# Kernel tuning notes

Hardware: AMD Instinct MI355X
Metric: run time of the kernel (lower is better)

## Reference

```python
import jax, jax.numpy as jnp
import numpy as np

V_MAX = 3.0
FEATURE_CLAMP = 10.0
TOP_K = 1


def _green_diag(d):
    """Diagonal of G = (tridiag(sub=1, diag=d, super=1))^{-1} for each batch row.
    d: (B, N) complex64. Stable two-sided continued-fraction (Thomas-like) recurrences:
      L_i = d_i - 1/L_{i-1},  U_i = d_i - 1/U_{i+1},  G_ii = 1/(L_i + U_i - d_i).
    Sequential over N (vectorized over B) via lax.scan.
    """
    dT = d.T  # (N, B)

    def step(c, di):
        nc = di - 1.0 / c
        return nc, nc

    L0 = dT[0]
    _, Lr = jax.lax.scan(step, L0, dT[1:])
    L = jnp.concatenate([L0[None], Lr], axis=0)  # (N, B)

    dR = dT[::-1]
    U0 = dR[0]
    _, Ur = jax.lax.scan(step, U0, dR[1:])
    U = jnp.concatenate([U0[None], Ur], axis=0)[::-1]  # (N, B)

    return (1.0 / (L + U - dT)).T  # (B, N)


def setup_inputs() -> dict:
    key = jax.random.key(0)
    B, N, D, E, F = 4, 4096, 512, 4, 2048
    ks = jax.random.split(key, 8)
    s = lambda k, sh, sc: (jax.random.normal(k, sh, jnp.float32) * sc)
    return dict(
        x=jax.random.normal(ks[0], (B, N, D), jnp.float32),
        v_proj_w=s(ks[1], (1, D), D ** -0.5),
        v_proj_b=jnp.zeros((1,), jnp.float32),
        gamma=jnp.float32(0.0),
        epsilon_param=jnp.float32(1.0),
        gate_w=s(ks[2], (E, D), D ** -0.5),
        gate_b=jnp.zeros((E,), jnp.float32),
        w1=s(ks[3], (E, D, F), D ** -0.5),
        b1=jnp.zeros((E, F), jnp.float32),
        w2=s(ks[4], (E, F, D), F ** -0.5),
        b2=jnp.zeros((E, D), jnp.float32),
        out_w=s(ks[5], (D, 2), 0.5),
        out_b=jnp.zeros((D,), jnp.float32),
        bk_scale=jnp.ones((D,), jnp.float32),
    )


def reference(x, v_proj_w, v_proj_b, gamma, epsilon_param, gate_w, gate_b,
              w1, b1, w2, b2, out_w, out_b, bk_scale):
    # 1) scalar potential from tokens
    v = jnp.einsum('bnd,od->bno', x, v_proj_w)[..., 0] + v_proj_b[0]  # (B, N)
    v = jnp.clip(v, -V_MAX, V_MAX)

    # 2) gamma-shifted complex tridiagonal Green's function diagonal
    eps = jax.nn.softplus(epsilon_param) + 1e-6
    z = 1j * (eps + gamma)                       # complex64 scalar
    d = ((v - 2.0).astype(jnp.complex64) - z)    # he_diag - z, (B, N)
    G = _green_diag(d)                            # (B, N) complex
    feats = jnp.clip(jnp.stack([G.real, G.imag], axis=-1), -FEATURE_CLAMP, FEATURE_CLAMP)  # (B,N,2)

    # 3) sparse MoE FFN (top-1 routing, experts = Linear -> GELU -> Linear)
    logits = jnp.einsum('bnd,ed->bne', x, gate_w) + gate_b
    probs = jax.nn.softmax(logits, axis=-1)
    top_p, top_i = jax.lax.top_k(probs, TOP_K)
    top_w = top_p / jnp.sum(top_p, axis=-1, keepdims=True)
    wmask = jnp.sum(jax.nn.one_hot(top_i, probs.shape[-1], dtype=probs.dtype) * top_w[..., None], axis=-2)  # (B,N,E)

    h = jax.nn.gelu(jnp.einsum('bnd,edf->benf', x, w1) + b1[None, :, None, :], approximate=False)
    y = jnp.einsum('benf,efd->bend', h, w2) + b2[None, :, None, :]
    ffn_out = jnp.einsum('bne,bend->bnd', wmask, y)

    # 4) combine spectral features with FFN output
    spec_out = jnp.einsum('bnc,dc->bnd', feats, out_w) + out_b
    return ffn_out + bk_scale * spec_out
```

## Files before the change

kernel.cpp:

```cpp
#include <hip/hip_runtime.h>
#include <hip/hip_bf16.h>
#include <math.h>


typedef __bf16 bf16x8 __attribute__((ext_vector_type(8)));
typedef float  f32x4  __attribute__((ext_vector_type(4)));
typedef __attribute__((address_space(3))) __bf16 lbf16;

#define B_   4
#define N_   4096
#define D_   512
#define E_   4
#define F_   2048
#define T_   (B_*N_)
#define CAP_ T_
#define R256 68
#define RT128 (R256*2)
#define PADROWS (R256*256)

#define LGKM_BARRIER() asm volatile("s_waitcnt lgkmcnt(0)\n\ts_barrier" ::: "memory")

__device__ __forceinline__ void gload_lds16(const __bf16* g, lbf16* l) {
    __builtin_amdgcn_global_load_lds(
        (__attribute__((address_space(1))) void*)(void*)g,
        (__attribute__((address_space(3))) void*)l, 16, 0, 0);
}

__device__ __forceinline__ float fast_gelu(float x) {
    float u = 1.5957691216f * fmaf(0.044715f * x, x * x, x);
    return x / (1.0f + __expf(-u));
}

__device__ __forceinline__ void mfma_tile(const char* Ab, const char* Bb,
                                          int cs0, int cs1, f32x4 acc[4][4]) {
    #pragma unroll
    for (int ks = 0; ks < 2; ++ks) {
        int cs = ks ? cs1 : cs0;
        bf16x8 af[4], bfr[4];
        #pragma unroll
        for (int m = 0; m < 4; ++m)
            af[m] = *(const bf16x8*)(Ab + m * 2048 + cs);
        #pragma unroll
        for (int n = 0; n < 4; ++n)
            bfr[n] = *(const bf16x8*)(Bb + n * 2048 + cs);
        #pragma unroll
        for (int m = 0; m < 4; ++m)
            #pragma unroll
            for (int n = 0; n < 4; ++n)
                acc[m][n] = __builtin_amdgcn_mfma_f32_16x16x32_bf16(af[m], bfr[n], acc[m][n], 0, 0, 0);
    }
}

__device__ alignas(256) __bf16 s_w1t[(size_t)E_*F_*D_];
__device__ alignas(256) __bf16 s_w2t[(size_t)E_*D_*F_];
__device__ alignas(256) __bf16 s_xb[(size_t)PADROWS*D_];
__device__ alignas(256) __bf16 s_H[(size_t)PADROWS*F_];
__device__ alignas(256) float2 s_d[T_];
__device__ alignas(256) float2 s_feats[T_];
__device__ alignas(256) float2 s_L[T_];
__device__ alignas(256) float2 s_U[T_];
__device__ alignas(256) int    s_perm[E_*CAP_];
__device__ alignas(256) int    s_cnt[E_];
__device__ alignas(256) int    s_tpre[8];
__device__ alignas(256) int    s_eid[T_];

__global__ void transpose_bf16_kernel(const float* __restrict__ src,
                                      __bf16* __restrict__ dst,
                                      int R, int C) {
    __shared__ alignas(16) float tile[32][33];
    int e = blockIdx.z;
    const float* s = src + (size_t)e * R * C;
    __bf16*      d = dst + (size_t)e * R * C;
    int c0 = blockIdx.x * 32, r0 = blockIdx.y * 32;
    int tx = threadIdx.x, ty = threadIdx.y;
    #pragma unroll
    for (int i = 0; i < 4; ++i)
        tile[ty + i*8][tx] = s[(size_t)(r0 + ty + i*8) * C + c0 + tx];
    __syncthreads();
    #pragma unroll
    for (int i = 0; i < 4; ++i)
        d[(size_t)(c0 + ty + i*8) * R + r0 + tx] = (__bf16)tile[tx][ty + i*8];
}

__device__ inline float dot8(float4 a, float4 b, float4 c, float4 d) {
    float s =      a.x * c.x;
    s = fmaf(a.y, c.y, s); s = fmaf(a.z, c.z, s); s = fmaf(a.w, c.w, s);
    s = fmaf(b.x, d.x, s); s = fmaf(b.y, d.y, s); s = fmaf(b.z, d.z, s);
    s = fmaf(b.w, d.w, s);
    return s;
}

__device__ inline float wave_sum(float s) {
    #pragma unroll
    for (int off = 32; off > 0; off >>= 1) s += __shfl_xor(s, off);
    return s;
}

__global__ __launch_bounds__(256) void prep_kernel(
        const float* __restrict__ x,
        const float* __restrict__ vw, const float* __restrict__ vb,
        const float* __restrict__ gamma, const float* __restrict__ epsp,
        const float* __restrict__ gw, const float* __restrict__ gb,
        float2* __restrict__ dbuf, int* __restrict__ eid) {
    int wv = threadIdx.x >> 6, lane = threadIdx.x & 63;
    int token = blockIdx.x * 4 + wv;
    const float4* xr = (const float4*)(x + (size_t)token * D_);
    float4 xa = xr[lane*2], xb = xr[lane*2 + 1];

    const float4* vr = (const float4*)vw;
    float sv = dot8(xa, xb, vr[lane*2], vr[lane*2 + 1]);
    float sg0, sg1, sg2, sg3;
    {
        const float4* g0 = (const float4*)(gw + 0*D_);
        const float4* g1 = (const float4*)(gw + 1*D_);
        const float4* g2 = (const float4*)(gw + 2*D_);
        const float4* g3 = (const float4*)(gw + 3*D_);
        sg0 = dot8(xa, xb, g0[lane*2], g0[lane*2+1]);
        sg1 = dot8(xa, xb, g1[lane*2], g1[lane*2+1]);
        sg2 = dot8(xa, xb, g2[lane*2], g2[lane*2+1]);
        sg3 = dot8(xa, xb, g3[lane*2], g3[lane*2+1]);
    }
    sv  = wave_sum(sv);
    sg0 = wave_sum(sg0); sg1 = wave_sum(sg1);
    sg2 = wave_sum(sg2); sg3 = wave_sum(sg3);

    if (lane == 0) {
        float v = sv + vb[0];
        v = fminf(fmaxf(v, -3.0f), 3.0f);
        float eps = log1pf(expf(epsp[0])) + 1e-6f;
        dbuf[token] = make_float2(v - 2.0f, -(eps + gamma[0]));

        float l0 = sg0 + gb[0], l1 = sg1 + gb[1], l2 = sg2 + gb[2], l3 = sg3 + gb[3];
        float best = l0; int be = 0;
        if (l1 > best) { best = l1; be = 1; }
        if (l2 > best) { best = l2; be = 2; }
        if (l3 > best) { best = l3; be = 3; }
        eid[token] = be;
    }
}

__global__ __launch_bounds__(1024) void route_kernel(
        const int* __restrict__ eid, int* __restrict__ perm,
        int* __restrict__ cnt, int* __restrict__ tpre) {
    __shared__ int chunkcnt[256][4];
    __shared__ int chunkoff[256][4];
    __shared__ int totals[4];
    int tid = threadIdx.x;
    int wv = tid >> 6, lane = tid & 63;

    for (int c = wv; c < 256; c += 16) {
        int e = eid[c * 64 + lane];
        unsigned long long m0 = __ballot(e == 0);
        unsigned long long m1 = __ballot(e == 1);
        unsigned long long m2 = __ballot(e == 2);
        unsigned long long m3 = __ballot(e == 3);
        if (lane == 0) {
            chunkcnt[c][0] = __popcll(m0);
            chunkcnt[c][1] = __popcll(m1);
            chunkcnt[c][2] = __popcll(m2);
            chunkcnt[c][3] = __popcll(m3);
        }
    }
    __syncthreads();

    if (wv < 4) {
        int e = wv, carry = 0;
        #pragma unroll
        for (int g = 0; g < 4; ++g) {
            int idx = g * 64 + lane;
            int v = chunkcnt[idx][e];
            int s = v;
            #pragma unroll
            for (int off = 1; off < 64; off <<= 1) {
                int u = __shfl_up(s, off);
                if (lane >= off) s += u;
            }
            chunkoff[idx][e] = carry + s - v;
            carry += __shfl(s, 63);
        }
        if (lane == 0) { cnt[e] = carry; totals[e] = carry; }
    }
    __syncthreads();
    if (tid == 0) {
        int acc = 0;
        #pragma unroll
        for (int e = 0; e < E_; ++e) { tpre[e] = acc; acc += (totals[e] + 255) >> 8; }
        tpre[4] = acc;
    }

    for (int c = wv; c < 256; c += 16) {
        int t = c * 64 + lane;
        int e = eid[t];
        unsigned long long m0 = __ballot(e == 0);
        unsigned long long m1 = __ballot(e == 1);
        unsigned long long m2 = __ballot(e == 2);
        unsigned long long m3 = __ballot(e == 3);
        unsigned long long mym = (e == 0) ? m0 : (e == 1) ? m1 : (e == 2) ? m2 : m3;
        unsigned long long below = lane ? (mym & ((1ull << lane) - 1ull)) : 0ull;
        int pos = chunkoff[c][e] + __popcll(below);
        perm[e * CAP_ + pos] = t;
    }
}

__global__ __launch_bounds__(512) void scan_kernel(
        const float2* __restrict__ dbuf, float2* __restrict__ Lb,
        float2* __restrict__ Ub, float2* __restrict__ feats) {
    __shared__ alignas(16) float chunkM[8][64][8];
    __shared__ alignas(16) float bound[8][64][4];
    int tid = threadIdx.x;
    int s = tid >> 6, c = tid & 63;
    int b = s & 3, dir = s >> 2;

    {
        float ar=1, ai=0, br=0, bi=0, cr=0, ci=0, dr=1, di=0;
        for (int j = 0; j < 64; ++j) {
            int seq = c*64 + j;
            int orig = dir ? (N_-1 - seq) : seq;
            float2 dv = dbuf[b*N_ + orig];
            float nar = dv.x*ar - dv.y*ai - cr;
            float nai = dv.x*ai + dv.y*ar - ci;
            float nbr = dv.x*br - dv.y*bi - dr;
            float nbi = dv.x*bi + dv.y*br - di;
            cr = ar; ci = ai; dr = br; di = bi;
            ar = nar; ai = nai; br = nbr; bi = nbi;
            if ((j & 7) == 7) {
                float m = fmaxf(fmaxf(fmaxf(fabsf(ar),fabsf(ai)),fmaxf(fabsf(br),fabsf(bi))),
                                fmaxf(fmaxf(fabsf(cr),fabsf(ci)),fmaxf(fabsf(dr),fabsf(di))));
                float inv = 1.0f / fmaxf(m, 1e-30f);
                ar*=inv; ai*=inv; br*=inv; bi*=inv; cr*=inv; ci*=inv; dr*=inv; di*=inv;
            }
        }
        float* cm = chunkM[s][c];
        cm[0]=ar; cm[1]=ai; cm[2]=br; cm[3]=bi; cm[4]=cr; cm[5]=ci; cm[6]=dr; cm[7]=di;
    }
    __syncthreads();

    if (tid < 8) {
        int ss = tid;
        float pr=1, pi=0, qr=0, qi=0;
        for (int cc = 0; cc < 64; ++cc) {
            float* bd = bound[ss][cc];
            bd[0]=pr; bd[1]=pi; bd[2]=qr; bd[3]=qi;
            const float* m = chunkM[ss][cc];
            float npr = m[0]*pr - m[1]*pi + m[2]*qr - m[3]*qi;
            float npi = m[0]*pi + m[1]*pr + m[2]*qi + m[3]*qr;
            float nqr = m[4]*pr - m[5]*pi + m[6]*qr - m[7]*qi;
            float nqi = m[4]*pi + m[5]*pr + m[6]*qi + m[7]*qr;
            float mx = fmaxf(fmaxf(fabsf(npr),fabsf(npi)), fmaxf(fabsf(nqr),fabsf(nqi)));
            float inv = 1.0f / fmaxf(mx, 1e-30f);
            pr = npr*inv; pi = npi*inv; qr = nqr*inv; qi = nqi*inv;
        }
    }
    __syncthreads();

    {
        const float* bd = bound[s][c];
        float pr=bd[0], pi=bd[1], qr=bd[2], qi=bd[3];
        float den = fmaxf(pr*pr + pi*pi, 1e-30f);
        float invr = (qr*pr + qi*pi) / den;
        float invi = (qi*pr - qr*pi) / den;
        for (int j = 0; j < 64; ++j) {
            int seq = c*64 + j;
            int orig = dir ? (N_-1 - seq) : seq;
            int t = b*N_ + orig;
            float2 dv = dbuf[t];
            float Lr = dv.x - invr, Li = dv.y - invi;
            if (dir) Ub[t] = make_float2(Lr, Li);
            else     Lb[t] = make_float2(Lr, Li);
            float d2 = Lr*Lr + Li*Li;
            invr = Lr / d2; invi = -Li / d2;
        }
    }
    __threadfence();
    __syncthreads();

    for (int t = tid; t < T_; t += 512) {
        float2 L = Lb[t], U = Ub[t], dv = dbuf[t];
        float sr = L.x + U.x - dv.x;
        float si = L.y + U.y - dv.y;
        float den = sr*sr + si*si;
        float Gr = sr / den, Gi = -si / den;
        Gr = fminf(fmaxf(Gr, -10.0f), 10.0f);
        Gi = fminf(fmaxf(Gi, -10.0f), 10.0f);
        feats[t] = make_float2(Gr, Gi);
    }
}

__global__ __launch_bounds__(256) void reorder_kernel(
        const float* __restrict__ x, const int* __restrict__ perm,
        const int* __restrict__ cnt, const int* __restrict__ tpre,
        __bf16* __restrict__ xb) {
    int wv = threadIdx.x >> 6, lane = threadIdx.x & 63;
    int prow = blockIdx.x * 4 + wv;
    if (prow >= tpre[4] * 256) return;
    int e = 0;
    #pragma unroll
    for (int k = 1; k < E_; ++k) if (prow >= tpre[k] * 256) e = k;
    int i = prow - tpre[e] * 256;
    int token = (i < cnt[e]) ? perm[e * CAP_ + i] : -1;
    bf16x8 v = {0,0,0,0,0,0,0,0};
    if (token >= 0) {
        const float4* xr = (const float4*)(x + (size_t)token * D_);
        float4 a = xr[lane*2], b = xr[lane*2 + 1];
        v = (bf16x8){(__bf16)a.x,(__bf16)a.y,(__bf16)a.z,(__bf16)a.w,
                     (__bf16)b.x,(__bf16)b.y,(__bf16)b.z,(__bf16)b.w};
    }
    *(bf16x8*)(xb + (size_t)prow * D_ + lane * 8) = v;
}

__global__ __launch_bounds__(512, 4) void gemm1_kernel(
        const __bf16* __restrict__ xb, const __bf16* __restrict__ w1t,
        const float* __restrict__ b1, __bf16* __restrict__ Hb,
        const int* __restrict__ tpre) {
    int bid = blockIdx.x;
    int lb  = (bid & 7) * 136 + (bid >> 3);
    int rt = lb >> 4, ct = lb & 15;
    if (rt >= tpre[4]) return;
    int e = 0;
    #pragma unroll
    for (int k = 1; k < E_; ++k) if (rt >= tpre[k]) e = k;

    __shared__ __bf16 A[256 * 64];
    __shared__ __bf16 Bm[128 * 64];

    int tid = threadIdx.x, lane = tid & 63, wv = tid >> 6;
    int fl = lane & 15, gl = lane >> 4;
    int wr = wv >> 1, wc = wv & 1;

    int r8    = lane >> 3;
    int scolb = ((lane & 7) * 16) ^ (r8 << 4);
    const __bf16* aS0 = xb  + (size_t)(rt * 256 + wv * 32 + r8) * 512 + (scolb >> 1);
    const __bf16* bS0 = w1t + (size_t)(e * F_ + ct * 128 + wv * 16 + r8) * 512 + (scolb >> 1);
    lbf16* aD0 = (lbf16*)A  + wv * 32 * 64;
    lbf16* bD0 = (lbf16*)Bm + wv * 16 * 64;

    int xorv = (fl & 7) << 4;
    int cs0 = (gl * 16) ^ xorv;
    int cs1 = (64 + gl * 16) ^ xorv;
    const char* Ab = (const char*)A  + (wr * 64 + fl) * 128;
    const char* Bb = (const char*)Bm + (wc * 64 + fl) * 128;

    f32x4 acc[4][4];
    #pragma unroll
    for (int m = 0; m < 4; ++m)
        #pragma unroll
        for (int n = 0; n < 4; ++n) acc[m][n] = (f32x4){0.f,0.f,0.f,0.f};

    #pragma unroll
    for (int i = 0; i < 4; ++i)
        gload_lds16(aS0 + (size_t)i * 8 * 512, aD0 + i * 512);
    #pragma unroll
    for (int i = 0; i < 2; ++i)
        gload_lds16(bS0 + (size_t)i * 8 * 512, bD0 + i * 512);

    for (int kt = 0; kt < 8; ++kt) {
        __syncthreads();
        mfma_tile(Ab, Bb, cs0, cs1, acc);
        if (kt + 1 < 8) {
            LGKM_BARRIER();
            #pragma unroll
            for (int i = 0; i < 4; ++i)
                gload_lds16(aS0 + (size_t)i * 8 * 512 + (kt + 1) * 64, aD0 + i * 512);
            #pragma unroll
            for (int i = 0; i < 2; ++i)
                gload_lds16(bS0 + (size_t)i * 8 * 512 + (kt + 1) * 64, bD0 + i * 512);
        }
    }

    int gre = rt * 256 + wr * 64;
    int gce = ct * 128 + wc * 64;
    float b1v[4];
    #pragma unroll
    for (int n = 0; n < 4; ++n) b1v[n] = b1[e * F_ + gce + n*16 + fl];
    #pragma unroll
    for (int m = 0; m < 4; ++m)
        #pragma unroll
        for (int r = 0; r < 4; ++r) {
            __bf16* hrow = Hb + (size_t)(gre + m*16 + gl*4 + r) * F_ + gce;
            #pragma unroll
            for (int n = 0; n < 4; ++n)
                hrow[n*16 + fl] = (__bf16)fast_gelu(acc[m][n][r] + b1v[n]);
        }
}

__global__ __launch_bounds__(256, 4) void gemm2_kernel(
        const __bf16* __restrict__ Hb, const __bf16* __restrict__ w2t,
        const float* __restrict__ b2, const float* __restrict__ outw,
        const float* __restrict__ outb, const float* __restrict__ bk,
        const float2* __restrict__ feats, const int* __restrict__ perm,
        const int* __restrict__ cnt_p, const int* __restrict__ tpre,
        float* __restrict__ out) {
    int bid = blockIdx.x;
    int lb  = (bid & 7) * 68 + (bid >> 3);
    int rt = lb >> 2, ct = lb & 3;
    if (rt >= tpre[4] * 2) return;
    int e = 0;
    #pragma unroll
    for (int k = 1; k < E_; ++k) if (rt >= tpre[k] * 2) e = k;

    __shared__ __bf16 A[128 * 64];
    __shared__ __bf16 Bm[128 * 64];

    int tid = threadIdx.x, lane = tid & 63, wv = tid >> 6;
    int fl = lane & 15, gl = lane >> 4;
    int wr = wv >> 1, wc = wv & 1;

    int r0    = wv * 8 + (lane >> 3);
    int scolb = ((lane & 7) * 16) ^ ((lane >> 3) << 4);
    const __bf16* aS0 = Hb  + (size_t)(rt * 128 + r0) * F_ + (scolb >> 1);
    const __bf16* bS0 = w2t + (size_t)(e * D_ + ct * 128 + r0) * F_ + (scolb >> 1);
    lbf16* aD0 = (lbf16*)A  + wv * 512;
    lbf16* bD0 = (lbf16*)Bm + wv * 512;

    int xorv = (fl & 7) << 4;
    int cs0 = (gl * 16) ^ xorv;
    int cs1 = (64 + gl * 16) ^ xorv;
    const char* Ab = (const char*)A  + (wr * 64 + fl) * 128;
    const char* Bb = (const char*)Bm + (wc * 64 + fl) * 128;

    f32x4 acc[4][4];
    #pragma unroll
    for (int m = 0; m < 4; ++m)
        #pragma unroll
        for (int n = 0; n < 4; ++n) acc[m][n] = (f32x4){0.f,0.f,0.f,0.f};

    #pragma unroll
    for (int i = 0; i < 4; ++i) {
        gload_lds16(aS0 + (size_t)i * 32 * F_, aD0 + i * 2048);
        gload_lds16(bS0 + (size_t)i * 32 * F_, bD0 + i * 2048);
    }
    for (int kt = 0; kt < 32; ++kt) {
        __syncthreads();
        mfma_tile(Ab, Bb, cs0, cs1, acc);
        if (kt + 1 < 32) {
            LGKM_BARRIER();
            #pragma unroll
            for (int i = 0; i < 4; ++i) {
                gload_lds16(aS0 + (size_t)i * 32 * F_ + (kt + 1) * 64, aD0 + i * 2048);
                gload_lds16(bS0 + (size_t)i * 32 * F_ + (kt + 1) * 64, bD0 + i * 2048);
            }
        }
    }

    int cnt = cnt_p[e];
    int ibase = rt * 128 + wr * 64 - tpre[e] * 256;
    int gce = ct * 128 + wc * 64;
    float c_b2[4], c_o0[4], c_o1[4], c_ob[4], c_bk[4];
    #pragma unroll
    for (int n = 0; n < 4; ++n) {
        int dcol = gce + n*16 + fl;
        c_b2[n] = b2[e * D_ + dcol];
        c_o0[n] = outw[dcol * 2 + 0];
        c_o1[n] = outw[dcol * 2 + 1];
        c_ob[n] = outb[dcol];
        c_bk[n] = bk[dcol];
    }
    #pragma unroll
    for (int m = 0; m < 4; ++m)
        #pragma unroll
        for (int r = 0; r < 4; ++r) {
            int i = ibase + m*16 + gl*4 + r;
            if (i >= cnt) continue;
            int token = perm[e * CAP_ + i];
            float2 ft = feats[token];
            float* orow = out + (size_t)token * D_;
            #pragma unroll
            for (int n = 0; n < 4; ++n) {
                int dcol = gce + n*16 + fl;
                float spec = ft.x * c_o0[n] + ft.y * c_o1[n] + c_ob[n];
                orow[dcol] = acc[m][n][r] + c_b2[n] + c_bk[n] * spec;
            }
        }
}

extern "C" void kernel_launch(void* const* d_in, const int* in_sizes, int n_in,
                              void* d_out, int out_size, void* d_ws, size_t ws_size,
                              hipStream_t stream) {
    const float* x     = (const float*)d_in[0];
    const float* vpw   = (const float*)d_in[1];
    const float* vpb   = (const float*)d_in[2];
    const float* gamma = (const float*)d_in[3];
    const float* epsp  = (const float*)d_in[4];
    const float* gw    = (const float*)d_in[5];
    const float* gb    = (const float*)d_in[6];
    const float* w1    = (const float*)d_in[7];
    const float* b1    = (const float*)d_in[8];
    const float* w2    = (const float*)d_in[9];
    const float* b2    = (const float*)d_in[10];
    const float* ow    = (const float*)d_in[11];
    const float* ob    = (const float*)d_in[12];
    const float* bk    = (const float*)d_in[13];
    float* out = (float*)d_out;

    const size_t szW  = (size_t)E_ * F_ * D_ * sizeof(__bf16);
    const size_t szF2 = (size_t)T_ * sizeof(float2);
    const size_t szPm = (size_t)E_ * CAP_ * sizeof(int);
    const size_t szCt = 256;
    const size_t szXb = (size_t)PADROWS * D_ * sizeof(__bf16);
    const size_t szH  = (size_t)PADROWS * F_ * sizeof(__bf16);
    const size_t szEi = (size_t)T_ * sizeof(int);
    size_t need = 2*szW + 4*szF2 + szPm + 2*szCt + szXb + szH + szEi + 16*256;

    __bf16 *w1t, *w2t, *xbuf, *Hbuf; float2 *dbuf, *Lb, *Ub, *feats;
    int *perm, *cnt, *tpre, *eid;
    int use_ws = (d_ws != nullptr && ws_size >= need);
    if (use_ws) {
        size_t off = 0;
        auto carve = [&](size_t bytes) {
            void* p = (char*)d_ws + off;
            off += (bytes + 255) & ~(size_t)255;
            return p;
        };
        w1t   = (__bf16*)carve(szW);
        w2t   = (__bf16*)carve(szW);
        xbuf  = (__bf16*)carve(szXb);
        Hbuf  = (__bf16*)carve(szH);
        dbuf  = (float2*)carve(szF2);
        Lb    = (float2*)carve(szF2);
        Ub    = (float2*)carve(szF2);
        feats = (float2*)carve(szF2);
        perm  = (int*)   carve(szPm);
        cnt   = (int*)   carve(szCt);
        tpre  = (int*)   carve(szCt);
        eid   = (int*)   carve(szEi);
    } else {
        void* p;
        hipGetSymbolAddress(&p, HIP_SYMBOL(s_w1t));  w1t   = (__bf16*)p;
        hipGetSymbolAddress(&p, HIP_SYMBOL(s_w2t));  w2t   = (__bf16*)p;
        hipGetSymbolAddress(&p, HIP_SYMBOL(s_xb));   xbuf  = (__bf16*)p;
        hipGetSymbolAddress(&p, HIP_SYMBOL(s_H));    Hbuf  = (__bf16*)p;
        hipGetSymbolAddress(&p, HIP_SYMBOL(s_d));    dbuf  = (float2*)p;
        hipGetSymbolAddress(&p, HIP_SYMBOL(s_L));    Lb    = (float2*)p;
        hipGetSymbolAddress(&p, HIP_SYMBOL(s_U));    Ub    = (float2*)p;
        hipGetSymbolAddress(&p, HIP_SYMBOL(s_feats));feats = (float2*)p;
        hipGetSymbolAddress(&p, HIP_SYMBOL(s_perm)); perm  = (int*)p;
        hipGetSymbolAddress(&p, HIP_SYMBOL(s_cnt));  cnt   = (int*)p;
        hipGetSymbolAddress(&p, HIP_SYMBOL(s_tpre)); tpre  = (int*)p;
        hipGetSymbolAddress(&p, HIP_SYMBOL(s_eid));  eid   = (int*)p;
    }

    dim3 tb(32, 8);
    transpose_bf16_kernel<<<dim3(F_/32, D_/32, E_), tb, 0, stream>>>(w1, w1t, D_, F_);
    transpose_bf16_kernel<<<dim3(D_/32, F_/32, E_), tb, 0, stream>>>(w2, w2t, F_, D_);
    prep_kernel<<<T_/4, 256, 0, stream>>>(x, vpw, vpb, gamma, epsp, gw, gb, dbuf, eid);
    route_kernel<<<1, 1024, 0, stream>>>(eid, perm, cnt, tpre);
    scan_kernel<<<1, 512, 0, stream>>>(dbuf, Lb, Ub, feats);
    reorder_kernel<<<PADROWS/4, 256, 0, stream>>>(x, perm, cnt, tpre, xbuf);
    gemm1_kernel<<<R256*16, 512, 0, stream>>>(xbuf, w1t, b1, Hbuf, tpre);
    gemm2_kernel<<<RT128*4, 256, 0, stream>>>(Hbuf, w2t, b2, ow, ob, bk,
                                              feats, perm, cnt, tpre, out);
}
```

Baseline: 231.2 us.

## Enlarge gemm2 tile to 256 rows, merge transposes and route/scan launches

gemm2 now uses 512-thread blocks that compute 256x128 output tiles instead of 128x128, which halves redundant loads of the w2t operand and halves the number of blocks. The two weight transposes become one launch, and the routing and tridiagonal scan kernels become one two-block launch so they run concurrently. This cuts launch overhead and serialization, but the larger gemm2 tile uses more LDS and registers per block and gives fewer blocks for load balance.

After: 217.5 us. 5.9% less time.

```diff
diff --git a/kernel.cpp b/kernel.cpp
--- a/kernel.cpp
+++ b/kernel.cpp
@@ -15,7 +15,6 @@
 #define T_   (B_*N_)
 #define CAP_ T_
 #define R256 68
-#define RT128 (R256*2)
 #define PADROWS (R256*256)
 
 #define LGKM_BARRIER() asm volatile("s_waitcnt lgkmcnt(0)\n\ts_barrier" ::: "memory")
@@ -64,14 +63,23 @@
 __device__ alignas(256) int    s_tpre[8];
 __device__ alignas(256) int    s_eid[T_];
 
-__global__ void transpose_bf16_kernel(const float* __restrict__ src,
-                                      __bf16* __restrict__ dst,
-                                      int R, int C) {
+__global__ void transpose_both_kernel(const float* __restrict__ w1,
+                                      const float* __restrict__ w2,
+                                      __bf16* __restrict__ w1t,
+                                      __bf16* __restrict__ w2t) {
     __shared__ alignas(16) float tile[32][33];
-    int e = blockIdx.z;
-    const float* s = src + (size_t)e * R * C;
-    __bf16*      d = dst + (size_t)e * R * C;
-    int c0 = blockIdx.x * 32, r0 = blockIdx.y * 32;
+    int idx = blockIdx.x;
+    int which = idx >> 12;
+    int r = idx & 4095;
+    int e = r >> 10;
+    int t = r & 1023;
+    int R, C, c0, r0;
+    const float* s;
+    __bf16* d;
+    if (which == 0) { R = D_; C = F_; c0 = (t & 63) * 32; r0 = (t >> 6) * 32;
+                      s = w1 + (size_t)e * R * C; d = w1t + (size_t)e * R * C; }
+    else            { R = F_; C = D_; c0 = (t & 15) * 32; r0 = (t >> 4) * 32;
+                      s = w2 + (size_t)e * R * C; d = w2t + (size_t)e * R * C; }
     int tx = threadIdx.x, ty = threadIdx.y;
     #pragma unroll
     for (int i = 0; i < 4; ++i)
@@ -139,150 +147,149 @@
     }
 }
 
-__global__ __launch_bounds__(1024) void route_kernel(
+__global__ __launch_bounds__(1024) void route_scan_kernel(
         const int* __restrict__ eid, int* __restrict__ perm,
-        int* __restrict__ cnt, int* __restrict__ tpre) {
-    __shared__ int chunkcnt[256][4];
-    __shared__ int chunkoff[256][4];
-    __shared__ int totals[4];
-    int tid = threadIdx.x;
-    int wv = tid >> 6, lane = tid & 63;
-
-    for (int c = wv; c < 256; c += 16) {
-        int e = eid[c * 64 + lane];
-        unsigned long long m0 = __ballot(e == 0);
-        unsigned long long m1 = __ballot(e == 1);
-        unsigned long long m2 = __ballot(e == 2);
-        unsigned long long m3 = __ballot(e == 3);
-        if (lane == 0) {
-            chunkcnt[c][0] = __popcll(m0);
-            chunkcnt[c][1] = __popcll(m1);
-            chunkcnt[c][2] = __popcll(m2);
-            chunkcnt[c][3] = __popcll(m3);
-        }
-    }
-    __syncthreads();
-
-    if (wv < 4) {
-        int e = wv, carry = 0;
-        #pragma unroll
-        for (int g = 0; g < 4; ++g) {
-            int idx = g * 64 + lane;
-            int v = chunkcnt[idx][e];
-            int s = v;
-            #pragma unroll
-            for (int off = 1; off < 64; off <<= 1) {
-                int u = __shfl_up(s, off);
-                if (lane >= off) s += u;
-            }
-            chunkoff[idx][e] = carry + s - v;
-            carry += __shfl(s, 63);
-        }
-        if (lane == 0) { cnt[e] = carry; totals[e] = carry; }
-    }
-    __syncthreads();
-    if (tid == 0) {
-        int acc = 0;
-        #pragma unroll
-        for (int e = 0; e < E_; ++e) { tpre[e] = acc; acc += (totals[e] + 255) >> 8; }
-        tpre[4] = acc;
-    }
-
-    for (int c = wv; c < 256; c += 16) {
-        int t = c * 64 + lane;
-        int e = eid[t];
-        unsigned long long m0 = __ballot(e == 0);
-        unsigned long long m1 = __ballot(e == 1);
-        unsigned long long m2 = __ballot(e == 2);
-        unsigned long long m3 = __ballot(e == 3);
-        unsigned long long mym = (e == 0) ? m0 : (e == 1) ? m1 : (e == 2) ? m2 : m3;
-        unsigned long long below = lane ? (mym & ((1ull << lane) - 1ull)) : 0ull;
-        int pos = chunkoff[c][e] + __popcll(below);
-        perm[e * CAP_ + pos] = t;
-    }
-}
-
-__global__ __launch_bounds__(512) void scan_kernel(
+        int* __restrict__ cnt, int* __restrict__ tpre,
         const float2* __restrict__ dbuf, float2* __restrict__ Lb,
         float2* __restrict__ Ub, float2* __restrict__ feats) {
-    __shared__ alignas(16) float chunkM[8][64][8];
-    __shared__ alignas(16) float bound[8][64][4];
     int tid = threadIdx.x;
-    int s = tid >> 6, c = tid & 63;
-    int b = s & 3, dir = s >> 2;
-
-    {
-        float ar=1, ai=0, br=0, bi=0, cr=0, ci=0, dr=1, di=0;
-        for (int j = 0; j < 64; ++j) {
-            int seq = c*64 + j;
-            int orig = dir ? (N_-1 - seq) : seq;
-            float2 dv = dbuf[b*N_ + orig];
-            float nar = dv.x*ar - dv.y*ai - cr;
-            float nai = dv.x*ai + dv.y*ar - ci;
-            float nbr = dv.x*br - dv.y*bi - dr;
-            float nbi = dv.x*bi + dv.y*br - di;
-            cr = ar; ci = ai; dr = br; di = bi;
-            ar = nar; ai = nai; br = nbr; bi = nbi;
-            if ((j & 7) == 7) {
-                float m = fmaxf(fmaxf(fmaxf(fabsf(ar),fabsf(ai)),fmaxf(fabsf(br),fabsf(bi))),
-                                fmaxf(fmaxf(fabsf(cr),fabsf(ci)),fmaxf(fabsf(dr),fabsf(di))));
-                float inv = 1.0f / fmaxf(m, 1e-30f);
-                ar*=inv; ai*=inv; br*=inv; bi*=inv; cr*=inv; ci*=inv; dr*=inv; di*=inv;
+    if (blockIdx.x == 0) {
+        __shared__ int chunkcnt[256][4];
+        __shared__ int chunkoff[256][4];
+        __shared__ int totals[4];
+        int wv = tid >> 6, lane = tid & 63;
+
+        for (int c = wv; c < 256; c += 16) {
+            int e = eid[c * 64 + lane];
+            unsigned long long m0 = __ballot(e == 0);
+            unsigned long long m1 = __ballot(e == 1);
+            unsigned long long m2 = __ballot(e == 2);
+            unsigned long long m3 = __ballot(e == 3);
+            if (lane == 0) {
+                chunkcnt[c][0] = __popcll(m0);
+                chunkcnt[c][1] = __popcll(m1);
+                chunkcnt[c][2] = __popcll(m2);
+                chunkcnt[c][3] = __popcll(m3);
             }
         }
-        float* cm = chunkM[s][c];
-        cm[0]=ar; cm[1]=ai; cm[2]=br; cm[3]=bi; cm[4]=cr; cm[5]=ci; cm[6]=dr; cm[7]=di;
-    }
-    __syncthreads();
-
-    if (tid < 8) {
-        int ss = tid;
-        float pr=1, pi=0, qr=0, qi=0;
-        for (int cc = 0; cc < 64; ++cc) {
-            float* bd = bound[ss][cc];
-            bd[0]=pr; bd[1]=pi; bd[2]=qr; bd[3]=qi;
-            const float* m = chunkM[ss][cc];
-            float npr = m[0]*pr - m[1]*pi + m[2]*qr - m[3]*qi;
-            float npi = m[0]*pi + m[1]*pr + m[2]*qi + m[3]*qr;
-            float nqr = m[4]*pr - m[5]*pi + m[6]*qr - m[7]*qi;
-            float nqi = m[4]*pi + m[5]*pr + m[6]*qi + m[7]*qr;
-            float mx = fmaxf(fmaxf(fabsf(npr),fabsf(npi)), fmaxf(fabsf(nqr),fabsf(nqi)));
-            float inv = 1.0f / fmaxf(mx, 1e-30f);
-            pr = npr*inv; pi = npi*inv; qr = nqr*inv; qi = nqi*inv;
-        }
-    }
-    __syncthreads();
-
-    {
-        const float* bd = bound[s][c];
-        float pr=bd[0], pi=bd[1], qr=bd[2], qi=bd[3];
-        float den = fmaxf(pr*pr + pi*pi, 1e-30f);
-        float invr = (qr*pr + qi*pi) / den;
-        float invi = (qi*pr - qr*pi) / den;
-        for (int j = 0; j < 64; ++j) {
-            int seq = c*64 + j;
-            int orig = dir ? (N_-1 - seq) : seq;
-            int t = b*N_ + orig;
-            float2 dv = dbuf[t];
-            float Lr = dv.x - invr, Li = dv.y - invi;
-            if (dir) Ub[t] = make_float2(Lr, Li);
-            else     Lb[t] = make_float2(Lr, Li);
-            float d2 = Lr*Lr + Li*Li;
-            invr = Lr / d2; invi = -Li / d2;
-        }
-    }
-    __threadfence();
-    __syncthreads();
-
-    for (int t = tid; t < T_; t += 512) {
-        float2 L = Lb[t], U = Ub[t], dv = dbuf[t];
-        float sr = L.x + U.x - dv.x;
-        float si = L.y + U.y - dv.y;
-        float den = sr*sr + si*si;
-        float Gr = sr / den, Gi = -si / den;
-        Gr = fminf(fmaxf(Gr, -10.0f), 10.0f);
-        Gi = fminf(fmaxf(Gi, -10.0f), 10.0f);
-        feats[t] = make_float2(Gr, Gi);
+        __syncthreads();
+
+        if (wv < 4) {
+            int e = wv, carry = 0;
+            #pragma unroll
+            for (int g = 0; g < 4; ++g) {
+                int idx = g * 64 + lane;
+                int v = chunkcnt[idx][e];
+                int s = v;
+                #pragma unroll
+                for (int off = 1; off < 64; off <<= 1) {
+                    int u = __shfl_up(s, off);
+                    if (lane >= off) s += u;
+                }
+                chunkoff[idx][e] = carry + s - v;
+                carry += __shfl(s, 63);
+            }
+            if (lane == 0) { cnt[e] = carry; totals[e] = carry; }
+        }
+        __syncthreads();
+        if (tid == 0) {
+            int acc = 0;
+            #pragma unroll
+            for (int e = 0; e < E_; ++e) { tpre[e] = acc; acc += (totals[e] + 255) >> 8; }
+            tpre[4] = acc;
+        }
+
+        for (int c = wv; c < 256; c += 16) {
+            int t = c * 64 + lane;
+            int e = eid[t];
+            unsigned long long m0 = __ballot(e == 0);
+            unsigned long long m1 = __ballot(e == 1);
+            unsigned long long m2 = __ballot(e == 2);
+            unsigned long long m3 = __ballot(e == 3);
+            unsigned long long mym = (e == 0) ? m0 : (e == 1) ? m1 : (e == 2) ? m2 : m3;
+            unsigned long long below = lane ? (mym & ((1ull << lane) - 1ull)) : 0ull;
+            int pos = chunkoff[c][e] + __popcll(below);
+            perm[e * CAP_ + pos] = t;
+        }
+    } else {
+        __shared__ alignas(16) float chunkM[8][64][8];
+        __shared__ alignas(16) float bound[8][64][4];
+        int s = tid >> 6, c = tid & 63;
+        int b = s & 3, dir = (s >> 2) & 1;
+
+        if (tid < 512) {
+            float ar=1, ai=0, br=0, bi=0, cr=0, ci=0, dr=1, di=0;
+            for (int j = 0; j < 64; ++j) {
+                int seq = c*64 + j;
+                int orig = dir ? (N_-1 - seq) : seq;
+                float2 dv = dbuf[b*N_ + orig];
+                float nar = dv.x*ar - dv.y*ai - cr;
+                float nai = dv.x*ai + dv.y*ar - ci;
+                float nbr = dv.x*br - dv.y*bi - dr;
+                float nbi = dv.x*bi + dv.y*br - di;
+                cr = ar; ci = ai; dr = br; di = bi;
+                ar = nar; ai = nai; br = nbr; bi = nbi;
+                if ((j & 7) == 7) {
+                    float m = fmaxf(fmaxf(fmaxf(fabsf(ar),fabsf(ai)),fmaxf(fabsf(br),fabsf(bi))),
+                                    fmaxf(fmaxf(fabsf(cr),fabsf(ci)),fmaxf(fabsf(dr),fabsf(di))));
+                    float inv = 1.0f / fmaxf(m, 1e-30f);
+                    ar*=inv; ai*=inv; br*=inv; bi*=inv; cr*=inv; ci*=inv; dr*=inv; di*=inv;
+                }
+            }
+            float* cm = chunkM[s][c];
+            cm[0]=ar; cm[1]=ai; cm[2]=br; cm[3]=bi; cm[4]=cr; cm[5]=ci; cm[6]=dr; cm[7]=di;
+        }
+        __syncthreads();
+
+        if (tid < 8) {
+            int ss = tid;
+            float pr=1, pi=0, qr=0, qi=0;
+            for (int cc = 0; cc < 64; ++cc) {
+                float* bd = bound[ss][cc];
+                bd[0]=pr; bd[1]=pi; bd[2]=qr; bd[3]=qi;
+                const float* m = chunkM[ss][cc];
+                float npr = m[0]*pr - m[1]*pi + m[2]*qr - m[3]*qi;
+                float npi = m[0]*pi + m[1]*pr + m[2]*qi + m[3]*qr;
+                float nqr = m[4]*pr - m[5]*pi + m[6]*qr - m[7]*qi;
+                float nqi = m[4]*pi + m[5]*pr + m[6]*qi + m[7]*qr;
+                float mx = fmaxf(fmaxf(fabsf(npr),fabsf(npi)), fmaxf(fabsf(nqr),fabsf(nqi)));
+                float inv = 1.0f / fmaxf(mx, 1e-30f);
+                pr = npr*inv; pi = npi*inv; qr = nqr*inv; qi = nqi*inv;
+            }
+        }
+        __syncthreads();
+
+        if (tid < 512) {
+            const float* bd = bound[s][c];
+            float pr=bd[0], pi=bd[1], qr=bd[2], qi=bd[3];
+            float den = fmaxf(pr*pr + pi*pi, 1e-30f);
+            float invr = (qr*pr + qi*pi) / den;
+            float invi = (qi*pr - qr*pi) / den;
+            for (int j = 0; j < 64; ++j) {
+                int seq = c*64 + j;
+                int orig = dir ? (N_-1 - seq) : seq;
+                int t = b*N_ + orig;
+                float2 dv = dbuf[t];
+                float Lr = dv.x - invr, Li = dv.y - invi;
+                if (dir) Ub[t] = make_float2(Lr, Li);
+                else     Lb[t] = make_float2(Lr, Li);
+                float d2 = Lr*Lr + Li*Li;
+                invr = Lr / d2; invi = -Li / d2;
+            }
+        }
+        __threadfence();
+        __syncthreads();
+
+        for (int t = tid; t < T_; t += 1024) {
+            float2 L = Lb[t], U = Ub[t], dv = dbuf[t];
+            float sr = L.x + U.x - dv.x;
+            float si = L.y + U.y - dv.y;
+            float den = sr*sr + si*si;
+            float Gr = sr / den, Gi = -si / den;
+            Gr = fminf(fmaxf(Gr, -10.0f), 10.0f);
+            Gi = fminf(fmaxf(Gi, -10.0f), 10.0f);
+            feats[t] = make_float2(Gr, Gi);
+        }
     }
 }
 
@@ -383,7 +390,7 @@
         }
 }
 
-__global__ __launch_bounds__(256, 4) void gemm2_kernel(
+__global__ __launch_bounds__(512, 4) void gemm2_kernel(
         const __bf16* __restrict__ Hb, const __bf16* __restrict__ w2t,
         const float* __restrict__ b2, const float* __restrict__ outw,
         const float* __restrict__ outb, const float* __restrict__ bk,
@@ -391,26 +398,26 @@
         const int* __restrict__ cnt_p, const int* __restrict__ tpre,
         float* __restrict__ out) {
     int bid = blockIdx.x;
-    int lb  = (bid & 7) * 68 + (bid >> 3);
+    int lb  = (bid & 7) * 34 + (bid >> 3);
     int rt = lb >> 2, ct = lb & 3;
-    if (rt >= tpre[4] * 2) return;
+    if (rt >= tpre[4]) return;
     int e = 0;
     #pragma unroll
-    for (int k = 1; k < E_; ++k) if (rt >= tpre[k] * 2) e = k;
-
-    __shared__ __bf16 A[128 * 64];
+    for (int k = 1; k < E_; ++k) if (rt >= tpre[k]) e = k;
+
+    __shared__ __bf16 A[256 * 64];
     __shared__ __bf16 Bm[128 * 64];
 
     int tid = threadIdx.x, lane = tid & 63, wv = tid >> 6;
     int fl = lane & 15, gl = lane >> 4;
     int wr = wv >> 1, wc = wv & 1;
 
-    int r0    = wv * 8 + (lane >> 3);
-    int scolb = ((lane & 7) * 16) ^ ((lane >> 3) << 4);
-    const __bf16* aS0 = Hb  + (size_t)(rt * 128 + r0) * F_ + (scolb >> 1);
-    const __bf16* bS0 = w2t + (size_t)(e * D_ + ct * 128 + r0) * F_ + (scolb >> 1);
-    lbf16* aD0 = (lbf16*)A  + wv * 512;
-    lbf16* bD0 = (lbf16*)Bm + wv * 512;
+    int r8    = lane >> 3;
+    int scolb = ((lane & 7) * 16) ^ (r8 << 4);
+    const __bf16* aS0 = Hb  + (size_t)(rt * 256 + wv * 32 + r8) * F_ + (scolb >> 1);
+    const __bf16* bS0 = w2t + (size_t)(e * D_ + ct * 128 + wv * 16 + r8) * F_ + (scolb >> 1);
+    lbf16* aD0 = (lbf16*)A  + wv * 32 * 64;
+    lbf16* bD0 = (lbf16*)Bm + wv * 16 * 64;
 
     int xorv = (fl & 7) << 4;
     int cs0 = (gl * 16) ^ xorv;
@@ -425,25 +432,28 @@
         for (int n = 0; n < 4; ++n) acc[m][n] = (f32x4){0.f,0.f,0.f,0.f};
 
     #pragma unroll
-    for (int i = 0; i < 4; ++i) {
-        gload_lds16(aS0 + (size_t)i * 32 * F_, aD0 + i * 2048);
-        gload_lds16(bS0 + (size_t)i * 32 * F_, bD0 + i * 2048);
-    }
+    for (int i = 0; i < 4; ++i)
+        gload_lds16(aS0 + (size_t)i * 8 * F_, aD0 + i * 512);
+    #pragma unroll
+    for (int i = 0; i < 2; ++i)
+        gload_lds16(bS0 + (size_t)i * 8 * F_, bD0 + i * 512);
+
     for (int kt = 0; kt < 32; ++kt) {
         __syncthreads();
         mfma_tile(Ab, Bb, cs0, cs1, acc);
         if (kt + 1 < 32) {
             LGKM_BARRIER();
             #pragma unroll
-            for (int i = 0; i < 4; ++i) {
-                gload_lds16(aS0 + (size_t)i * 32 * F_ + (kt + 1) * 64, aD0 + i * 2048);
-                gload_lds16(bS0 + (size_t)i * 32 * F_ + (kt + 1) * 64, bD0 + i * 2048);
-            }
+            for (int i = 0; i < 4; ++i)
+                gload_lds16(aS0 + (size_t)i * 8 * F_ + (kt + 1) * 64, aD0 + i * 512);
+            #pragma unroll
+            for (int i = 0; i < 2; ++i)
+                gload_lds16(bS0 + (size_t)i * 8 * F_ + (kt + 1) * 64, bD0 + i * 512);
         }
     }
 
     int cnt = cnt_p[e];
-    int ibase = rt * 128 + wr * 64 - tpre[e] * 256;
+    int ibase = rt * 256 + wr * 64 - tpre[e] * 256;
     int gce = ct * 128 + wc * 64;
     float c_b2[4], c_o0[4], c_o1[4], c_ob[4], c_bk[4];
     #pragma unroll
@@ -540,13 +550,11 @@
     }
 
     dim3 tb(32, 8);
-    transpose_bf16_kernel<<<dim3(F_/32, D_/32, E_), tb, 0, stream>>>(w1, w1t, D_, F_);
-    transpose_bf16_kernel<<<dim3(D_/32, F_/32, E_), tb, 0, stream>>>(w2, w2t, F_, D_);
+    transpose_both_kernel<<<8192, tb, 0, stream>>>(w1, w2, w1t, w2t);
     prep_kernel<<<T_/4, 256, 0, stream>>>(x, vpw, vpb, gamma, epsp, gw, gb, dbuf, eid);
-    route_kernel<<<1, 1024, 0, stream>>>(eid, perm, cnt, tpre);
-    scan_kernel<<<1, 512, 0, stream>>>(dbuf, Lb, Ub, feats);
+    route_scan_kernel<<<2, 1024, 0, stream>>>(eid, perm, cnt, tpre, dbuf, Lb, Ub, feats);
     reorder_kernel<<<PADROWS/4, 256, 0, stream>>>(x, perm, cnt, tpre, xbuf);
     gemm1_kernel<<<R256*16, 512, 0, stream>>>(xbuf, w1t, b1, Hbuf, tpre);
-    gemm2_kernel<<<RT128*4, 256, 0, stream>>>(Hbuf, w2t, b2, ow, ob, bk,
-                                              feats, perm, cnt, tpre, out);
-}
+    gemm2_kernel<<<R256*4, 512, 0, stream>>>(Hbuf, w2t, b2, ow, ob, bk,
+                                             feats, perm, cnt, tpre, out);
+}
```
